# Kernel optimization log

Measured on AMD Instinct MI355X. Metric: run time of the kernel, lower is better.

## Reference

```python
import jax, jax.numpy as jnp
import numpy as np

B, T, E, H = 8, 2048, 1024, 128

def setup_inputs() -> dict:
    key = jax.random.key(0)
    kx, kq, kk, kv = jax.random.split(key, 4)
    x = jax.random.normal(kx, (B, T, E), dtype=jnp.float32)
    # Linear(E, H, bias=False) weights, stored as (E, H) so y = x @ W
    s = 1.0 / np.sqrt(E)
    Wq = jax.random.normal(kq, (E, H), dtype=jnp.float32) * s
    Wk = jax.random.normal(kk, (E, H), dtype=jnp.float32) * s
    Wv = jax.random.normal(kv, (E, H), dtype=jnp.float32) * s
    return {"x": x, "Wq": Wq, "Wk": Wk, "Wv": Wv}

def reference(x, Wq, Wk, Wv):
    # x: (B, T, E)
    Tcur = x.shape[1]
    q = jnp.einsum('bte,eh->bth', x, Wq)
    k = jnp.einsum('bte,eh->bth', x, Wk)
    v = jnp.einsum('bte,eh->bth', x, Wv)
    scores = jnp.einsum('bqh,bkh->bqk', q, k)  # (B, T, T)
    # NOTE: source multiplies by x.shape[2]**0.5 where x.shape[2] == T here
    scores = scores * jnp.sqrt(jnp.asarray(Tcur, dtype=scores.dtype))
    causal = jnp.tril(jnp.ones((Tcur, Tcur), dtype=bool))
    scores = jnp.where(causal, scores, -jnp.inf)
    attn = jax.nn.softmax(scores, axis=2)
    # dropout p=0.0 -> identity
    return jnp.einsum('bqk,bkh->bqh', attn, v)
```

## Files before the change

kernel.cpp:

```cpp
#include <hip/hip_runtime.h>
#include <hip/hip_bf16.h>
#include <math.h>

#define B_ 8
#define T_ 2048
#define E_ 1024
#define H_ 128
#define M_ (B_*T_)
#define SCALE_ 45.25483399593904f
#define SEG_ 4

typedef __attribute__((ext_vector_type(8))) short bf16x8;
typedef __attribute__((ext_vector_type(4))) float f32x4;

#define mfma16(A, Bv, C) __builtin_amdgcn_mfma_f32_16x16x32_bf16((A), (Bv), (C), 0, 0, 0)

#define FRAGW(g, kc, lane)  ((((size_t)(g)*32 + (kc))*64 + (lane))*8)
#define FRAGK(b, kt16, kc, lane) (((((size_t)(b)*128 + (kt16))*4 + (kc))*64 + (lane))*8)
#define FRAGV(b, ht, kt32, lane) (((((size_t)(b)*8 + (ht))*64 + (kt32))*64 + (lane))*8)

__device__ __forceinline__ ushort bf16_rne(float f) {
  unsigned u = __float_as_uint(f);
  u += 0x7fffu + ((u >> 16) & 1u);
  return (ushort)(u >> 16);
}
__device__ __forceinline__ float bf16_tof(ushort h) {
  return __uint_as_float(((unsigned)h) << 16);
}

__device__ __forceinline__ void lds_barrier() {
  asm volatile("s_waitcnt lgkmcnt(0)" ::: "memory");
  __builtin_amdgcn_s_barrier();
}

__global__ __launch_bounds__(256) void wsplit(
    const float* __restrict__ Wq, const float* __restrict__ Wk,
    const float* __restrict__ Wv,
    ushort* __restrict__ whT, ushort* __restrict__ wlT)
{
  const int idx  = blockIdx.x * 256 + threadIdx.x;
  const int mat  = idx >> 14;
  const int rem  = idx & 16383;
  const int nt   = rem >> 11;
  const int kc   = (rem >> 6) & 31;
  const int lane = rem & 63;
  const int quad = lane >> 4, l15 = lane & 15;
  const float* W = (mat == 0) ? Wq : (mat == 1) ? Wk : Wv;
  const int n  = nt * 16 + l15;
  const int k0 = kc * 32 + quad * 8;
  bf16x8 hv, lv;
  #pragma unroll
  for (int j = 0; j < 8; ++j) {
    const float f = W[(size_t)(k0 + j) * H_ + n];
    const ushort h = bf16_rne(f);
    hv[j] = (short)h;
    lv[j] = (short)bf16_rne(f - bf16_tof(h));
  }
  *(bf16x8*)(whT + (size_t)idx * 8) = hv;
  *(bf16x8*)(wlT + (size_t)idx * 8) = lv;
}

#define CVT8W(F0, F1, DSTOFF) do {                                            \
    const float f_[8] = {(F0).x, (F0).y, (F0).z, (F0).w,                      \
                         (F1).x, (F1).y, (F1).z, (F1).w};                     \
    bf16x8 hv_, lv_;                                                          \
    _Pragma("unroll")                                                         \
    for (int jj_ = 0; jj_ < 8; ++jj_) {                                       \
      const ushort h_ = bf16_rne(f_[jj_]);                                    \
      hv_[jj_] = (short)h_;                                                   \
      lv_[jj_] = (short)bf16_rne(f_[jj_] - bf16_tof(h_));                     \
    }                                                                         \
    *(bf16x8*)&SM[(DSTOFF) + ca * 8] = hv_;                                   \
    *(bf16x8*)&SM[(DSTOFF) + 2048 + ca * 8] = lv_;                            \
  } while (0)

#define AFRAG(CUR, HALFOFF, MT) \
    (*(const bf16x8*)&SM[(CUR)*8192 + (HALFOFF) + \
        (((MT)*4 + quad)*16 + (l15 ^ quad))*8])

#define PSTEP4(S, CUR, NXT, BHC, BLC, BHN, BLN) do {                          \
    bf16x8 ah_[4], al_[4];                                                    \
    _Pragma("unroll")                                                         \
    for (int mt_ = 0; mt_ < 4; ++mt_) {                                       \
      ah_[mt_] = AFRAG(CUR, 0,    mt_);                                       \
      al_[mt_] = AFRAG(CUR, 2048, mt_);                                       \
    }                                                                         \
    if ((S) + 1 < 16) {                                                       \
      _Pragma("unroll")                                                       \
      for (int kch_ = 0; kch_ < 2; ++kch_) {                                  \
        const int kcn_ = 2*((S)+1) + kch_;                                    \
        BHN[kch_*3+0] = *(const bf16x8*)(whT + FRAGW(gq,     kcn_, lane));    \
        BHN[kch_*3+1] = *(const bf16x8*)(whT + FRAGW(gq + 4, kcn_, lane));    \
        BHN[kch_*3+2] = *(const bf16x8*)(whT + FRAGW(gv,     kcn_, lane));    \
        BLN[kch_*2+0] = *(const bf16x8*)(wlT + FRAGW(gq,     kcn_, lane));    \
        BLN[kch_*2+1] = *(const bf16x8*)(wlT + FRAGW(gq + 4, kcn_, lane));    \
      }                                                                       \
    }                                                                         \
    float4 nx0_, nx1_, nx2_, nx3_;                                            \
    if ((S) + 2 < 16) {                                                       \
      nx0_ = *(const float4*)(xrow + 64*((S)+2));                             \
      nx1_ = *(const float4*)(xrow + 64*((S)+2) + 4);                         \
      nx2_ = *(const float4*)(xrow + 64*((S)+2) + 32);                        \
      nx3_ = *(const float4*)(xrow + 64*((S)+2) + 36);                        \
    } else { nx0_ = xf0; nx1_ = xf1; nx2_ = xf2; nx3_ = xf3; }                \
                                                     \
    __builtin_amdgcn_s_setprio(1);                                            \
    _Pragma("unroll")                                                         \
    for (int mt_ = 0; mt_ < 4; ++mt_) {                                       \
      acc[0][mt_] = mfma16(ah_[mt_], BHC[0], acc[0][mt_]);                    \
      acc[0][mt_] = mfma16(ah_[mt_], BLC[0], acc[0][mt_]);                    \
      acc[0][mt_] = mfma16(al_[mt_], BHC[0], acc[0][mt_]);                    \
      acc[1][mt_] = mfma16(ah_[mt_], BHC[1], acc[1][mt_]);                    \
      acc[1][mt_] = mfma16(ah_[mt_], BLC[1], acc[1][mt_]);                    \
      acc[1][mt_] = mfma16(al_[mt_], BHC[1], acc[1][mt_]);                    \
      acc[2][mt_] = mfma16(ah_[mt_], BHC[2], acc[2][mt_]);                    \
    }                                                                         \
    __builtin_amdgcn_s_setprio(0);                                            \
                                            \
    if ((S) + 1 < 16) {                                                       \
      CVT8W(xf0, xf1, (NXT)*8192);                                            \
      CVT8W(xf2, xf3, (NXT)*8192 + 4096);                                     \
    }                                                                         \
                                                \
    _Pragma("unroll")                                                         \
    for (int mt_ = 0; mt_ < 4; ++mt_) {                                       \
      ah_[mt_] = AFRAG(CUR, 4096, mt_);                                       \
      al_[mt_] = AFRAG(CUR, 6144, mt_);                                       \
    }                                                                         \
    __builtin_amdgcn_s_setprio(1);                                            \
    _Pragma("unroll")                                                         \
    for (int mt_ = 0; mt_ < 4; ++mt_) {                                       \
      acc[0][mt_] = mfma16(ah_[mt_], BHC[3], acc[0][mt_]);                    \
      acc[0][mt_] = mfma16(ah_[mt_], BLC[2], acc[0][mt_]);                    \
      acc[0][mt_] = mfma16(al_[mt_], BHC[3], acc[0][mt_]);                    \
      acc[1][mt_] = mfma16(ah_[mt_], BHC[4], acc[1][mt_]);                    \
      acc[1][mt_] = mfma16(ah_[mt_], BLC[3], acc[1][mt_]);                    \
      acc[1][mt_] = mfma16(al_[mt_], BHC[4], acc[1][mt_]);                    \
      acc[2][mt_] = mfma16(ah_[mt_], BHC[5], acc[2][mt_]);                    \
    }                                                                         \
    __builtin_amdgcn_s_setprio(0);                                            \
    xf0 = nx0_; xf1 = nx1_; xf2 = nx2_; xf3 = nx3_;                           \
    lds_barrier();                                                            \
  } while (0)

__global__ __launch_bounds__(256, 2) void proj_fused(
    const float* __restrict__ x,
    const ushort* __restrict__ whT, const ushort* __restrict__ wlT,
    ushort* __restrict__ qh, ushort* __restrict__ ql,
    ushort* __restrict__ kfh, ushort* __restrict__ kfl,
    ushort* __restrict__ vF)
{
  const int m0   = blockIdx.x * 64;
  const int half = blockIdx.y;
  const int tid  = threadIdx.x;
  const int wave = tid >> 6, lane = tid & 63;
  const int quad = lane >> 4, l15 = lane & 15;

  __shared__ __align__(16) ushort SM[16384];

  f32x4 acc[3][4];
  #pragma unroll
  for (int j = 0; j < 3; ++j)
    #pragma unroll
    for (int mt = 0; mt < 4; ++mt) acc[j][mt] = (f32x4){0.f, 0.f, 0.f, 0.f};

  const int arow  = tid >> 2;
  const int akoff = (tid & 3) * 8;
  const int ca    = ((arow >> 4) * 4 + (tid & 3)) * 16
                    + ((arow & 15) ^ (tid & 3));
  const int gq    = half * 8 + wave;
  const int gv    = 16 + half * 4 + wave;

  const float* xrow = x + (size_t)(m0 + arow) * E_ + akoff;

  float4 xf0, xf1, xf2, xf3;
  bf16x8 bhA[6], blA[4], bhB[6], blB[4];

  {
    const float4 a0 = *(const float4*)(xrow);
    const float4 a1 = *(const float4*)(xrow + 4);
    const float4 a2 = *(const float4*)(xrow + 32);
    const float4 a3 = *(const float4*)(xrow + 36);
    CVT8W(a0, a1, 0);
    CVT8W(a2, a3, 4096);
    xf0 = *(const float4*)(xrow + 64);
    xf1 = *(const float4*)(xrow + 68);
    xf2 = *(const float4*)(xrow + 96);
    xf3 = *(const float4*)(xrow + 100);
    #pragma unroll
    for (int kch = 0; kch < 2; ++kch) {
      bhA[kch*3+0] = *(const bf16x8*)(whT + FRAGW(gq,     kch, lane));
      bhA[kch*3+1] = *(const bf16x8*)(whT + FRAGW(gq + 4, kch, lane));
      bhA[kch*3+2] = *(const bf16x8*)(whT + FRAGW(gv,     kch, lane));
      blA[kch*2+0] = *(const bf16x8*)(wlT + FRAGW(gq,     kch, lane));
      blA[kch*2+1] = *(const bf16x8*)(wlT + FRAGW(gq + 4, kch, lane));
    }
  }
  lds_barrier();

  int s = 0;
  while (true) {
    PSTEP4(s, 0, 1, bhA, blA, bhB, blB); if (++s == 16) break;
    PSTEP4(s, 1, 0, bhB, blB, bhA, blA); if (++s == 16) break;
  }

  #pragma unroll
  for (int j = 0; j < 2; ++j) {
    const int g = gq + 4 * j;
    if (half == 0) {
      const int ncol = g * 16 + l15;
      #pragma unroll
      for (int mt = 0; mt < 4; ++mt)
        #pragma unroll
        for (int r = 0; r < 4; ++r) {
          const float a = acc[j][mt][r];
          const ushort h = bf16_rne(a);
          const size_t off = (size_t)(m0 + mt * 16 + quad * 4 + r) * H_ + ncol;
          qh[off] = h;
          ql[off] = bf16_rne(a - bf16_tof(h));
        }
    } else {
      const int hcol = (g - 8) * 16 + l15;
      const int kch  = hcol >> 5;
      const int qdh  = (hcol >> 3) & 3;
      const int jj   = hcol & 7;
      #pragma unroll
      for (int mt = 0; mt < 4; ++mt)
        #pragma unroll
        for (int r = 0; r < 4; ++r) {
          const float a = acc[j][mt][r];
          const int tg = m0 + mt * 16 + quad * 4 + r;
          const int bb = tg >> 11, tl = tg & 2047;
          const size_t ad = FRAGK(bb, tl >> 4, kch, qdh * 16 + (tl & 15)) + jj;
          const ushort h = bf16_rne(a);
          kfh[ad] = h;
          kfl[ad] = bf16_rne(a - bf16_tof(h));
        }
    }
  }
  __syncthreads();
  {
    ushort* smT = SM;
    const int lh = wave * 16 + l15;
    #pragma unroll
    for (int mt = 0; mt < 4; ++mt)
      #pragma unroll
      for (int r = 0; r < 4; ++r)
        smT[lh * 72 + mt * 16 + quad * 4 + r] = bf16_rne(acc[2][mt][r]);
    __syncthreads();
    const int bb = m0 >> 11, t0 = m0 & 2047;
    #pragma unroll
    for (int u = 0; u < 2; ++u) {
      const int c    = u * 256 + tid;
      const int lht  = c >> 7;
      const int ktl  = (c >> 6) & 1;
      const int lv   = c & 63;
      const int qv   = lv >> 4, l15v = lv & 15;
      *(bf16x8*)(vF + FRAGV(bb, half * 4 + lht, (t0 >> 5) + ktl, lv)) =
          *(const bf16x8*)&smT[(lht * 16 + l15v) * 72 + ktl * 32 + qv * 8];
    }
  }
}

__global__ __launch_bounds__(256) void attn_flash(
    const ushort* __restrict__ qh, const ushort* __restrict__ ql,
    const ushort* __restrict__ kfh, const ushort* __restrict__ kfl,
    const ushort* __restrict__ vF,
    ushort* __restrict__ Opart, float* __restrict__ mlpart)
{
  const int b    = (int)blockIdx.x & 7;
  const int seg  = (int)blockIdx.x >> 3;
  const int qt   = 31 - (int)blockIdx.y;
  const int q0   = qt * 64;
  const int tid  = threadIdx.x;
  const int wave = tid >> 6, lane = tid & 63;
  const int quad = lane >> 4, l15 = lane & 15;
  const f32x4 z4 = (f32x4){0.f, 0.f, 0.f, 0.f};

  __shared__ __align__(16) ushort SMa[12288];
  __shared__ __align__(16) unsigned smPw[1280];
  ushort* KhS = SMa;
  ushort* KlS = SMa + 4096;
  ushort* VtS = SMa + 8192;
  unsigned* pw = smPw + wave * 320;

  const int ntiles = 2 * qt + 2;
  const int cnt    = (ntiles + SEG_ - 1) >> 2;
  const int jt0    = seg * cnt;
  const int jt1    = (jt0 + cnt < ntiles) ? (jt0 + cnt) : ntiles;

  const int q0w = q0 + wave * 16;
  const int ntw = ((q0w + 15) >> 5) + 1;
  const size_t pidx = ((size_t)(b * 128 + qt * 4 + wave)) * SEG_ + seg;
  ushort* op = Opart + pidx * 2048;
  float*  ml = mlpart + pidx * 32;

  if (jt0 >= jt1) {
    const bf16x8 zz = {0, 0, 0, 0, 0, 0, 0, 0};
    #pragma unroll
    for (int u = 0; u < 4; ++u)
      *(bf16x8*)(op + lane * 32 + u * 8) = zz;
    if (lane < 32) ml[lane] = (lane & 1) ? 0.f : -1e30f;
    return;
  }

  const size_t base = (size_t)b * T_ * H_;

  const ushort* qhp = qh + base + (size_t)(q0w + l15) * H_ + quad * 8;
  const ushort* qlp = ql + base + (size_t)(q0w + l15) * H_ + quad * 8;
  bf16x8 Qh[4], Ql[4];
  #pragma unroll
  for (int c = 0; c < 4; ++c) {
    Qh[c] = *(const bf16x8*)(qhp + c * 32);
    Ql[c] = *(const bf16x8*)(qlp + c * 32);
  }

  f32x4 O[8];
  #pragma unroll
  for (int i = 0; i < 8; ++i) O[i] = z4;
  float mst = -1e30f;
  float lst = 0.f;

  bf16x8 rkh[2], rkl[2], rv[2];
  {
    #pragma unroll
    for (int u = 0; u < 2; ++u) {
      const int c = u * 256 + tid;
      rkh[u] = *(const bf16x8*)(kfh + FRAGK(b, 2 * jt0 + (c >> 8), (c >> 6) & 3, c & 63));
      rkl[u] = *(const bf16x8*)(kfl + FRAGK(b, 2 * jt0 + (c >> 8), (c >> 6) & 3, c & 63));
      rv[u]  = *(const bf16x8*)(vF  + FRAGV(b, c >> 6, jt0, c & 63));
    }
  }

  for (int jt = jt0; jt < jt1; ++jt) {
    __syncthreads();
    #pragma unroll
    for (int u = 0; u < 2; ++u) {
      const int c = u * 256 + tid;
      *(bf16x8*)&KhS[c * 8] = rkh[u];
      *(bf16x8*)&KlS[c * 8] = rkl[u];
      *(bf16x8*)&VtS[c * 8] = rv[u];
    }
    __syncthreads();

    if (jt + 1 < jt1) {
      #pragma unroll
      for (int u = 0; u < 2; ++u) {
        const int c = u * 256 + tid;
        rkh[u] = *(const bf16x8*)(kfh + FRAGK(b, 2 * (jt + 1) + (c >> 8), (c >> 6) & 3, c & 63));
        rkl[u] = *(const bf16x8*)(kfl + FRAGK(b, 2 * (jt + 1) + (c >> 8), (c >> 6) & 3, c & 63));
        rv[u]  = *(const bf16x8*)(vF  + FRAGV(b, c >> 6, jt + 1, c & 63));
      }
    }

    if (jt < ntw) {
      const int k0 = jt * 32;
      f32x4 shh0 = z4, shh1 = z4, sx0 = z4, sx1 = z4;
      #pragma unroll
      for (int c = 0; c < 4; ++c) {
        const bf16x8 kh0 = *(const bf16x8*)&KhS[(c * 64 + lane) * 8];
        const bf16x8 kh1 = *(const bf16x8*)&KhS[((4 + c) * 64 + lane) * 8];
        const bf16x8 kl0 = *(const bf16x8*)&KlS[(c * 64 + lane) * 8];
        const bf16x8 kl1 = *(const bf16x8*)&KlS[((4 + c) * 64 + lane) * 8];
        shh0 = mfma16(kh0, Qh[c], shh0);
        shh1 = mfma16(kh1, Qh[c], shh1);
        sx0  = mfma16(kl0, Qh[c], sx0);
        sx1  = mfma16(kl1, Qh[c], sx1);
        sx0  = mfma16(kh0, Ql[c], sx0);
        sx1  = mfma16(kh1, Ql[c], sx1);
      }

      float r0[4], r1[4];
      #pragma unroll
      for (int r = 0; r < 4; ++r) {
        r0[r] = shh0[r] + sx0[r];
        r1[r] = shh1[r] + sx1[r];
      }
      if (jt == ntw - 1) {
        const int base0 = q0w + l15 - k0 - quad * 4;
        #pragma unroll
        for (int r = 0; r < 4; ++r) {
          if (r > base0)      r0[r] = -1e30f;
          if (r > base0 - 16) r1[r] = -1e30f;
        }
      }

      float pm = fmaxf(fmaxf(fmaxf(r0[0], r0[1]), fmaxf(r0[2], r0[3])),
                       fmaxf(fmaxf(r1[0], r1[1]), fmaxf(r1[2], r1[3])));
      pm = fmaxf(pm, __shfl_xor(pm, 16));
      pm = fmaxf(pm, __shfl_xor(pm, 32));

      const float mnew  = fmaxf(mst, pm);
      const float alpha = __expf((mst - mnew) * SCALE_);
      mst = mnew;

      float p0[4], p1[4];
      #pragma unroll
      for (int r = 0; r < 4; ++r) {
        p0[r] = __expf((r0[r] - mnew) * SCALE_);
        p1[r] = __expf((r1[r] - mnew) * SCALE_);
      }
      float sm = ((p0[0] + p0[1]) + (p0[2] + p0[3])) +
                 ((p1[0] + p1[1]) + (p1[2] + p1[3]));
      sm += __shfl_xor(sm, 16);
      sm += __shfl_xor(sm, 32);
      lst = lst * alpha + sm;

      const unsigned w0 = (unsigned)bf16_rne(p0[0]) | ((unsigned)bf16_rne(p0[1]) << 16);
      const unsigned w1 = (unsigned)bf16_rne(p0[2]) | ((unsigned)bf16_rne(p0[3]) << 16);
      const unsigned w2 = (unsigned)bf16_rne(p1[0]) | ((unsigned)bf16_rne(p1[1]) << 16);
      const unsigned w3 = (unsigned)bf16_rne(p1[2]) | ((unsigned)bf16_rne(p1[3]) << 16);
      *(unsigned long long*)&pw[l15 * 20 + 2 * quad] =
          (unsigned long long)w0 | ((unsigned long long)w1 << 32);
      *(unsigned long long*)&pw[l15 * 20 + 8 + 2 * quad] =
          (unsigned long long)w2 | ((unsigned long long)w3 << 32);

      #pragma unroll
      for (int ct = 0; ct < 8; ++ct) {
        O[ct][0] *= alpha; O[ct][1] *= alpha;
        O[ct][2] *= alpha; O[ct][3] *= alpha;
      }
      const bf16x8 pB = *(const bf16x8*)&pw[l15 * 20 + 4 * quad];
      #pragma unroll
      for (int ct = 0; ct < 8; ++ct) {
        const bf16x8 vf = *(const bf16x8*)&VtS[(ct * 64 + lane) * 8];
        O[ct] = mfma16(vf, pB, O[ct]);
      }
    }
  }

  __syncthreads();
  {
    ushort* smO = SMa + wave * 2176;
    #pragma unroll
    for (int ct = 0; ct < 8; ++ct)
      #pragma unroll
      for (int r = 0; r < 4; ++r)
        smO[l15 * 136 + ct * 16 + quad * 4 + r] = bf16_rne(O[ct][r]);
    #pragma unroll
    for (int u = 0; u < 4; ++u) {
      const int q_ = u * 4 + quad;
      *(bf16x8*)(op + q_ * 128 + l15 * 8) =
          *(const bf16x8*)&smO[q_ * 136 + l15 * 8];
    }
  }
  if (quad == 0) {
    ml[l15 * 2]     = mst * SCALE_;
    ml[l15 * 2 + 1] = lst;
  }
}

__global__ __launch_bounds__(256) void attn_combine(
    const ushort* __restrict__ Opart, const float* __restrict__ mlpart,
    float* __restrict__ out)
{
  const int idx = blockIdx.x * 256 + threadIdx.x;
  const int c4  = idx & 31;
  const int r   = idx >> 5;
  const int t   = r & 2047;
  const int qt  = t >> 4, r16 = t & 15;
  const size_t pb = ((size_t)((r >> 11) * 128 + qt)) * SEG_;

  float m[SEG_], l[SEG_];
  #pragma unroll
  for (int s = 0; s < SEG_; ++s) {
    m[s] = mlpart[(pb + s) * 32 + r16 * 2];
    l[s] = mlpart[(pb + s) * 32 + r16 * 2 + 1];
  }
  float M = m[0];
  #pragma unroll
  for (int s = 1; s < SEG_; ++s) M = fmaxf(M, m[s]);
  float w[SEG_], L = 0.f;
  #pragma unroll
  for (int s = 0; s < SEG_; ++s) {
    w[s] = __expf(m[s] - M);
    L += l[s] * w[s];
  }
  float4 acc = make_float4(0.f, 0.f, 0.f, 0.f);
  #pragma unroll
  for (int s = 0; s < SEG_; ++s) {
    const ushort4 o = *(const ushort4*)(Opart + (pb + s) * 2048 + r16 * 128 + c4 * 4);
    acc.x += w[s] * bf16_tof(o.x);
    acc.y += w[s] * bf16_tof(o.y);
    acc.z += w[s] * bf16_tof(o.z);
    acc.w += w[s] * bf16_tof(o.w);
  }
  const float inv = 1.0f / L;
  *(float4*)(out + (size_t)r * H_ + c4 * 4) =
      make_float4(acc.x * inv, acc.y * inv, acc.z * inv, acc.w * inv);
}

extern "C" void kernel_launch(void* const* d_in, const int* in_sizes, int n_in,
                              void* d_out, int out_size, void* d_ws, size_t ws_size,
                              hipStream_t stream) {
  (void)in_sizes; (void)n_in; (void)out_size; (void)ws_size;
  const float* x  = (const float*)d_in[0];
  const float* Wq = (const float*)d_in[1];
  const float* Wk = (const float*)d_in[2];
  const float* Wv = (const float*)d_in[3];
  float* out = (float*)d_out;

  ushort* qhb = (ushort*)d_ws;
  ushort* qlb = qhb + (size_t)M_ * H_;
  ushort* kfh = qlb + (size_t)M_ * H_;
  ushort* kfl = kfh + (size_t)M_ * H_;
  ushort* vFb = kfl + (size_t)M_ * H_;
  ushort* whT = vFb + (size_t)M_ * H_;
  ushort* wlT = whT + (size_t)3 * H_ * E_;
  ushort* Opart = wlT + (size_t)3 * H_ * E_;
  float*  mlpart = (float*)(Opart + (size_t)B_ * 128 * SEG_ * 2048);

  wsplit<<<dim3(192), 256, 0, stream>>>(Wq, Wk, Wv, whT, wlT);
  proj_fused<<<dim3(M_/64, 2), 256, 0, stream>>>(x, whT, wlT,
                                                 qhb, qlb, kfh, kfl, vFb);
  attn_flash<<<dim3(B_*SEG_, 32), 256, 0, stream>>>(qhb, qlb, kfh, kfl, vFb,
                                                    Opart, mlpart);
  attn_combine<<<dim3(2048), 256, 0, stream>>>(Opart, mlpart, out);
}
```

Measured before the change: 170.0 us.

## Fuse split-KV combine into attention kernel via last-block atomic counter

Removes the separate attn_combine launch. Each attention block now fences its partial output, bumps a per-(batch, query-tile) atomic counter, and the last of the SEG_ segment blocks merges the partials and writes the final output. The counters are zeroed in the wsplit kernel. This saves one kernel launch and lets combine work overlap with other blocks, at the cost of a threadfence and atomic per block and serial combine work in the last-arriving block.

```diff
diff --git a/kernel.cpp b/kernel.cpp
--- a/kernel.cpp
+++ b/kernel.cpp
@@ -36,8 +36,10 @@
 __global__ __launch_bounds__(256) void wsplit(
     const float* __restrict__ Wq, const float* __restrict__ Wk,
     const float* __restrict__ Wv,
-    ushort* __restrict__ whT, ushort* __restrict__ wlT)
+    ushort* __restrict__ whT, ushort* __restrict__ wlT,
+    unsigned* __restrict__ cnt)
 {
+  if (blockIdx.x == 0) cnt[threadIdx.x] = 0u;
   const int idx  = blockIdx.x * 256 + threadIdx.x;
   const int mat  = idx >> 14;
   const int rem  = idx & 16383;
@@ -103,7 +105,6 @@
       nx2_ = *(const float4*)(xrow + 64*((S)+2) + 32);                        \
       nx3_ = *(const float4*)(xrow + 64*((S)+2) + 36);                        \
     } else { nx0_ = xf0; nx1_ = xf1; nx2_ = xf2; nx3_ = xf3; }                \
-                                                     \
     __builtin_amdgcn_s_setprio(1);                                            \
     _Pragma("unroll")                                                         \
     for (int mt_ = 0; mt_ < 4; ++mt_) {                                       \
@@ -116,12 +117,10 @@
       acc[2][mt_] = mfma16(ah_[mt_], BHC[2], acc[2][mt_]);                    \
     }                                                                         \
     __builtin_amdgcn_s_setprio(0);                                            \
-                                            \
     if ((S) + 1 < 16) {                                                       \
       CVT8W(xf0, xf1, (NXT)*8192);                                            \
       CVT8W(xf2, xf3, (NXT)*8192 + 4096);                                     \
     }                                                                         \
-                                                \
     _Pragma("unroll")                                                         \
     for (int mt_ = 0; mt_ < 4; ++mt_) {                                       \
       ah_[mt_] = AFRAG(CUR, 4096, mt_);                                       \
@@ -266,7 +265,8 @@
     const ushort* __restrict__ qh, const ushort* __restrict__ ql,
     const ushort* __restrict__ kfh, const ushort* __restrict__ kfl,
     const ushort* __restrict__ vF,
-    ushort* __restrict__ Opart, float* __restrict__ mlpart)
+    ushort* __restrict__ Opart, float* __restrict__ mlpart,
+    float* __restrict__ out, unsigned* __restrict__ cnt)
 {
   const int b    = (int)blockIdx.x & 7;
   const int seg  = (int)blockIdx.x >> 3;
@@ -279,15 +279,16 @@
 
   __shared__ __align__(16) ushort SMa[12288];
   __shared__ __align__(16) unsigned smPw[1280];
+  __shared__ int lastFlag;
   ushort* KhS = SMa;
   ushort* KlS = SMa + 4096;
   ushort* VtS = SMa + 8192;
   unsigned* pw = smPw + wave * 320;
 
   const int ntiles = 2 * qt + 2;
-  const int cnt    = (ntiles + SEG_ - 1) >> 2;
-  const int jt0    = seg * cnt;
-  const int jt1    = (jt0 + cnt < ntiles) ? (jt0 + cnt) : ntiles;
+  const int cntseg = (ntiles + SEG_ - 1) >> 2;
+  const int jt0    = seg * cntseg;
+  const int jt1    = (jt0 + cntseg < ntiles) ? (jt0 + cntseg) : ntiles;
 
   const int q0w = q0 + wave * 16;
   const int ntw = ((q0w + 15) >> 5) + 1;
@@ -301,193 +302,200 @@
     for (int u = 0; u < 4; ++u)
       *(bf16x8*)(op + lane * 32 + u * 8) = zz;
     if (lane < 32) ml[lane] = (lane & 1) ? 0.f : -1e30f;
-    return;
-  }
-
-  const size_t base = (size_t)b * T_ * H_;
-
-  const ushort* qhp = qh + base + (size_t)(q0w + l15) * H_ + quad * 8;
-  const ushort* qlp = ql + base + (size_t)(q0w + l15) * H_ + quad * 8;
-  bf16x8 Qh[4], Ql[4];
-  #pragma unroll
-  for (int c = 0; c < 4; ++c) {
-    Qh[c] = *(const bf16x8*)(qhp + c * 32);
-    Ql[c] = *(const bf16x8*)(qlp + c * 32);
-  }
-
-  f32x4 O[8];
-  #pragma unroll
-  for (int i = 0; i < 8; ++i) O[i] = z4;
-  float mst = -1e30f;
-  float lst = 0.f;
-
-  bf16x8 rkh[2], rkl[2], rv[2];
-  {
-    #pragma unroll
-    for (int u = 0; u < 2; ++u) {
-      const int c = u * 256 + tid;
-      rkh[u] = *(const bf16x8*)(kfh + FRAGK(b, 2 * jt0 + (c >> 8), (c >> 6) & 3, c & 63));
-      rkl[u] = *(const bf16x8*)(kfl + FRAGK(b, 2 * jt0 + (c >> 8), (c >> 6) & 3, c & 63));
-      rv[u]  = *(const bf16x8*)(vF  + FRAGV(b, c >> 6, jt0, c & 63));
-    }
-  }
-
-  for (int jt = jt0; jt < jt1; ++jt) {
-    __syncthreads();
-    #pragma unroll
-    for (int u = 0; u < 2; ++u) {
-      const int c = u * 256 + tid;
-      *(bf16x8*)&KhS[c * 8] = rkh[u];
-      *(bf16x8*)&KlS[c * 8] = rkl[u];
-      *(bf16x8*)&VtS[c * 8] = rv[u];
-    }
-    __syncthreads();
-
-    if (jt + 1 < jt1) {
+  } else {
+    const size_t base = (size_t)b * T_ * H_;
+
+    const ushort* qhp = qh + base + (size_t)(q0w + l15) * H_ + quad * 8;
+    const ushort* qlp = ql + base + (size_t)(q0w + l15) * H_ + quad * 8;
+    bf16x8 Qh[4], Ql[4];
+    #pragma unroll
+    for (int c = 0; c < 4; ++c) {
+      Qh[c] = *(const bf16x8*)(qhp + c * 32);
+      Ql[c] = *(const bf16x8*)(qlp + c * 32);
+    }
+
+    f32x4 O[8];
+    #pragma unroll
+    for (int i = 0; i < 8; ++i) O[i] = z4;
+    float mst = -1e30f;
+    float lst = 0.f;
+
+    bf16x8 rkh[2], rkl[2], rv[2];
+    {
       #pragma unroll
       for (int u = 0; u < 2; ++u) {
         const int c = u * 256 + tid;
-        rkh[u] = *(const bf16x8*)(kfh + FRAGK(b, 2 * (jt + 1) + (c >> 8), (c >> 6) & 3, c & 63));
-        rkl[u] = *(const bf16x8*)(kfl + FRAGK(b, 2 * (jt + 1) + (c >> 8), (c >> 6) & 3, c & 63));
-        rv[u]  = *(const bf16x8*)(vF  + FRAGV(b, c >> 6, jt + 1, c & 63));
-      }
-    }
-
-    if (jt < ntw) {
-      const int k0 = jt * 32;
-      f32x4 shh0 = z4, shh1 = z4, sx0 = z4, sx1 = z4;
-      #pragma unroll
-      for (int c = 0; c < 4; ++c) {
-        const bf16x8 kh0 = *(const bf16x8*)&KhS[(c * 64 + lane) * 8];
-        const bf16x8 kh1 = *(const bf16x8*)&KhS[((4 + c) * 64 + lane) * 8];
-        const bf16x8 kl0 = *(const bf16x8*)&KlS[(c * 64 + lane) * 8];
-        const bf16x8 kl1 = *(const bf16x8*)&KlS[((4 + c) * 64 + lane) * 8];
-        shh0 = mfma16(kh0, Qh[c], shh0);
-        shh1 = mfma16(kh1, Qh[c], shh1);
-        sx0  = mfma16(kl0, Qh[c], sx0);
-        sx1  = mfma16(kl1, Qh[c], sx1);
-        sx0  = mfma16(kh0, Ql[c], sx0);
-        sx1  = mfma16(kh1, Ql[c], sx1);
-      }
-
-      float r0[4], r1[4];
-      #pragma unroll
-      for (int r = 0; r < 4; ++r) {
-        r0[r] = shh0[r] + sx0[r];
-        r1[r] = shh1[r] + sx1[r];
-      }
-      if (jt == ntw - 1) {
-        const int base0 = q0w + l15 - k0 - quad * 4;
+        rkh[u] = *(const bf16x8*)(kfh + FRAGK(b, 2 * jt0 + (c >> 8), (c >> 6) & 3, c & 63));
+        rkl[u] = *(const bf16x8*)(kfl + FRAGK(b, 2 * jt0 + (c >> 8), (c >> 6) & 3, c & 63));
+        rv[u]  = *(const bf16x8*)(vF  + FRAGV(b, c >> 6, jt0, c & 63));
+      }
+    }
+
+    for (int jt = jt0; jt < jt1; ++jt) {
+      __syncthreads();
+      #pragma unroll
+      for (int u = 0; u < 2; ++u) {
+        const int c = u * 256 + tid;
+        *(bf16x8*)&KhS[c * 8] = rkh[u];
+        *(bf16x8*)&KlS[c * 8] = rkl[u];
+        *(bf16x8*)&VtS[c * 8] = rv[u];
+      }
+      __syncthreads();
+
+      if (jt + 1 < jt1) {
+        #pragma unroll
+        for (int u = 0; u < 2; ++u) {
+          const int c = u * 256 + tid;
+          rkh[u] = *(const bf16x8*)(kfh + FRAGK(b, 2 * (jt + 1) + (c >> 8), (c >> 6) & 3, c & 63));
+          rkl[u] = *(const bf16x8*)(kfl + FRAGK(b, 2 * (jt + 1) + (c >> 8), (c >> 6) & 3, c & 63));
+          rv[u]  = *(const bf16x8*)(vF  + FRAGV(b, c >> 6, jt + 1, c & 63));
+        }
+      }
+
+      if (jt < ntw) {
+        const int k0 = jt * 32;
+        f32x4 shh0 = z4, shh1 = z4, sx0 = z4, sx1 = z4;
+        #pragma unroll
+        for (int c = 0; c < 4; ++c) {
+          const bf16x8 kh0 = *(const bf16x8*)&KhS[(c * 64 + lane) * 8];
+          const bf16x8 kh1 = *(const bf16x8*)&KhS[((4 + c) * 64 + lane) * 8];
+          const bf16x8 kl0 = *(const bf16x8*)&KlS[(c * 64 + lane) * 8];
+          const bf16x8 kl1 = *(const bf16x8*)&KlS[((4 + c) * 64 + lane) * 8];
+          shh0 = mfma16(kh0, Qh[c], shh0);
+          shh1 = mfma16(kh1, Qh[c], shh1);
+          sx0  = mfma16(kl0, Qh[c], sx0);
+          sx1  = mfma16(kl1, Qh[c], sx1);
+          sx0  = mfma16(kh0, Ql[c], sx0);
+          sx1  = mfma16(kh1, Ql[c], sx1);
+        }
+
+        float r0[4], r1[4];
         #pragma unroll
         for (int r = 0; r < 4; ++r) {
-          if (r > base0)      r0[r] = -1e30f;
-          if (r > base0 - 16) r1[r] = -1e30f;
-        }
-      }
-
-      float pm = fmaxf(fmaxf(fmaxf(r0[0], r0[1]), fmaxf(r0[2], r0[3])),
-                       fmaxf(fmaxf(r1[0], r1[1]), fmaxf(r1[2], r1[3])));
-      pm = fmaxf(pm, __shfl_xor(pm, 16));
-      pm = fmaxf(pm, __shfl_xor(pm, 32));
-
-      const float mnew  = fmaxf(mst, pm);
-      const float alpha = __expf((mst - mnew) * SCALE_);
-      mst = mnew;
-
-      float p0[4], p1[4];
-      #pragma unroll
-      for (int r = 0; r < 4; ++r) {
-        p0[r] = __expf((r0[r] - mnew) * SCALE_);
-        p1[r] = __expf((r1[r] - mnew) * SCALE_);
-      }
-      float sm = ((p0[0] + p0[1]) + (p0[2] + p0[3])) +
-                 ((p1[0] + p1[1]) + (p1[2] + p1[3]));
-      sm += __shfl_xor(sm, 16);
-      sm += __shfl_xor(sm, 32);
-      lst = lst * alpha + sm;
-
-      const unsigned w0 = (unsigned)bf16_rne(p0[0]) | ((unsigned)bf16_rne(p0[1]) << 16);
-      const unsigned w1 = (unsigned)bf16_rne(p0[2]) | ((unsigned)bf16_rne(p0[3]) << 16);
-      const unsigned w2 = (unsigned)bf16_rne(p1[0]) | ((unsigned)bf16_rne(p1[1]) << 16);
-      const unsigned w3 = (unsigned)bf16_rne(p1[2]) | ((unsigned)bf16_rne(p1[3]) << 16);
-      *(unsigned long long*)&pw[l15 * 20 + 2 * quad] =
-          (unsigned long long)w0 | ((unsigned long long)w1 << 32);
-      *(unsigned long long*)&pw[l15 * 20 + 8 + 2 * quad] =
-          (unsigned long long)w2 | ((unsigned long long)w3 << 32);
-
-      #pragma unroll
-      for (int ct = 0; ct < 8; ++ct) {
-        O[ct][0] *= alpha; O[ct][1] *= alpha;
-        O[ct][2] *= alpha; O[ct][3] *= alpha;
-      }
-      const bf16x8 pB = *(const bf16x8*)&pw[l15 * 20 + 4 * quad];
-      #pragma unroll
-      for (int ct = 0; ct < 8; ++ct) {
-        const bf16x8 vf = *(const bf16x8*)&VtS[(ct * 64 + lane) * 8];
-        O[ct] = mfma16(vf, pB, O[ct]);
-      }
-    }
-  }
-
+          r0[r] = shh0[r] + sx0[r];
+          r1[r] = shh1[r] + sx1[r];
+        }
+        if (jt == ntw - 1) {
+          const int base0 = q0w + l15 - k0 - quad * 4;
+          #pragma unroll
+          for (int r = 0; r < 4; ++r) {
+            if (r > base0)      r0[r] = -1e30f;
+            if (r > base0 - 16) r1[r] = -1e30f;
+          }
+        }
+
+        float pm = fmaxf(fmaxf(fmaxf(r0[0], r0[1]), fmaxf(r0[2], r0[3])),
+                         fmaxf(fmaxf(r1[0], r1[1]), fmaxf(r1[2], r1[3])));
+        pm = fmaxf(pm, __shfl_xor(pm, 16));
+        pm = fmaxf(pm, __shfl_xor(pm, 32));
+
+        const float mnew  = fmaxf(mst, pm);
+        const float alpha = __expf((mst - mnew) * SCALE_);
+        mst = mnew;
+
+        float p0[4], p1[4];
+        #pragma unroll
+        for (int r = 0; r < 4; ++r) {
+          p0[r] = __expf((r0[r] - mnew) * SCALE_);
+          p1[r] = __expf((r1[r] - mnew) * SCALE_);
+        }
+        float sm = ((p0[0] + p0[1]) + (p0[2] + p0[3])) +
+                   ((p1[0] + p1[1]) + (p1[2] + p1[3]));
+        sm += __shfl_xor(sm, 16);
+        sm += __shfl_xor(sm, 32);
+        lst = lst * alpha + sm;
+
+        const unsigned w0 = (unsigned)bf16_rne(p0[0]) | ((unsigned)bf16_rne(p0[1]) << 16);
+        const unsigned w1 = (unsigned)bf16_rne(p0[2]) | ((unsigned)bf16_rne(p0[3]) << 16);
+        const unsigned w2 = (unsigned)bf16_rne(p1[0]) | ((unsigned)bf16_rne(p1[1]) << 16);
+        const unsigned w3 = (unsigned)bf16_rne(p1[2]) | ((unsigned)bf16_rne(p1[3]) << 16);
+        *(unsigned long long*)&pw[l15 * 20 + 2 * quad] =
+            (unsigned long long)w0 | ((unsigned long long)w1 << 32);
+        *(unsigned long long*)&pw[l15 * 20 + 8 + 2 * quad] =
+            (unsigned long long)w2 | ((unsigned long long)w3 << 32);
+
+        #pragma unroll
+        for (int ct = 0; ct < 8; ++ct) {
+          O[ct][0] *= alpha; O[ct][1] *= alpha;
+          O[ct][2] *= alpha; O[ct][3] *= alpha;
+        }
+        const bf16x8 pB = *(const bf16x8*)&pw[l15 * 20 + 4 * quad];
+        #pragma unroll
+        for (int ct = 0; ct < 8; ++ct) {
+          const bf16x8 vf = *(const bf16x8*)&VtS[(ct * 64 + lane) * 8];
+          O[ct] = mfma16(vf, pB, O[ct]);
+        }
+      }
+    }
+
+    __syncthreads();
+    {
+      ushort* smO = SMa + wave * 2176;
+      #pragma unroll
+      for (int ct = 0; ct < 8; ++ct)
+        #pragma unroll
+        for (int r = 0; r < 4; ++r)
+          smO[l15 * 136 + ct * 16 + quad * 4 + r] = bf16_rne(O[ct][r]);
+      #pragma unroll
+      for (int u = 0; u < 4; ++u) {
+        const int q_ = u * 4 + quad;
+        *(bf16x8*)(op + q_ * 128 + l15 * 8) =
+            *(const bf16x8*)&smO[q_ * 136 + l15 * 8];
+      }
+    }
+    if (quad == 0) {
+      ml[l15 * 2]     = mst * SCALE_;
+      ml[l15 * 2 + 1] = lst;
+    }
+  }
+
+  __threadfence();
   __syncthreads();
-  {
-    ushort* smO = SMa + wave * 2176;
-    #pragma unroll
-    for (int ct = 0; ct < 8; ++ct)
-      #pragma unroll
-      for (int r = 0; r < 4; ++r)
-        smO[l15 * 136 + ct * 16 + quad * 4 + r] = bf16_rne(O[ct][r]);
-    #pragma unroll
-    for (int u = 0; u < 4; ++u) {
-      const int q_ = u * 4 + quad;
-      *(bf16x8*)(op + q_ * 128 + l15 * 8) =
-          *(const bf16x8*)&smO[q_ * 136 + l15 * 8];
-    }
-  }
-  if (quad == 0) {
-    ml[l15 * 2]     = mst * SCALE_;
-    ml[l15 * 2 + 1] = lst;
-  }
-}
-
-__global__ __launch_bounds__(256) void attn_combine(
-    const ushort* __restrict__ Opart, const float* __restrict__ mlpart,
-    float* __restrict__ out)
-{
-  const int idx = blockIdx.x * 256 + threadIdx.x;
-  const int c4  = idx & 31;
-  const int r   = idx >> 5;
-  const int t   = r & 2047;
-  const int qt  = t >> 4, r16 = t & 15;
-  const size_t pb = ((size_t)((r >> 11) * 128 + qt)) * SEG_;
-
-  float m[SEG_], l[SEG_];
-  #pragma unroll
-  for (int s = 0; s < SEG_; ++s) {
-    m[s] = mlpart[(pb + s) * 32 + r16 * 2];
-    l[s] = mlpart[(pb + s) * 32 + r16 * 2 + 1];
-  }
-  float M = m[0];
-  #pragma unroll
-  for (int s = 1; s < SEG_; ++s) M = fmaxf(M, m[s]);
-  float w[SEG_], L = 0.f;
-  #pragma unroll
-  for (int s = 0; s < SEG_; ++s) {
-    w[s] = __expf(m[s] - M);
-    L += l[s] * w[s];
-  }
-  float4 acc = make_float4(0.f, 0.f, 0.f, 0.f);
-  #pragma unroll
-  for (int s = 0; s < SEG_; ++s) {
-    const ushort4 o = *(const ushort4*)(Opart + (pb + s) * 2048 + r16 * 128 + c4 * 4);
-    acc.x += w[s] * bf16_tof(o.x);
-    acc.y += w[s] * bf16_tof(o.y);
-    acc.z += w[s] * bf16_tof(o.z);
-    acc.w += w[s] * bf16_tof(o.w);
-  }
-  const float inv = 1.0f / L;
-  *(float4*)(out + (size_t)r * H_ + c4 * 4) =
-      make_float4(acc.x * inv, acc.y * inv, acc.z * inv, acc.w * inv);
+  if (tid == 0) {
+    const unsigned old = atomicAdd(&cnt[b * 32 + qt], 1u);
+    lastFlag = (old == SEG_ - 1) ? 1 : 0;
+  }
+  __syncthreads();
+  if (lastFlag) {
+    __threadfence();
+    #pragma unroll
+    for (int u = 0; u < 8; ++u) {
+      const int task = u * 256 + tid;
+      const int c4 = task & 31;
+      const int lr = task >> 5;
+      const int t  = qt * 64 + lr;
+      const int qt16 = t >> 4, r16 = t & 15;
+      const size_t pb = ((size_t)(b * 128 + qt16)) * SEG_;
+
+      float m[SEG_], l[SEG_];
+      #pragma unroll
+      for (int s = 0; s < SEG_; ++s) {
+        m[s] = mlpart[(pb + s) * 32 + r16 * 2];
+        l[s] = mlpart[(pb + s) * 32 + r16 * 2 + 1];
+      }
+      float M = m[0];
+      #pragma unroll
+      for (int s = 1; s < SEG_; ++s) M = fmaxf(M, m[s]);
+      float w[SEG_], L = 0.f;
+      #pragma unroll
+      for (int s = 0; s < SEG_; ++s) {
+        w[s] = __expf(m[s] - M);
+        L += l[s] * w[s];
+      }
+      float4 acc = make_float4(0.f, 0.f, 0.f, 0.f);
+      #pragma unroll
+      for (int s = 0; s < SEG_; ++s) {
+        const ushort4 o = *(const ushort4*)(Opart + (pb + s) * 2048 + r16 * 128 + c4 * 4);
+        acc.x += w[s] * bf16_tof(o.x);
+        acc.y += w[s] * bf16_tof(o.y);
+        acc.z += w[s] * bf16_tof(o.z);
+        acc.w += w[s] * bf16_tof(o.w);
+      }
+      const float inv = 1.0f / L;
+      *(float4*)(out + ((size_t)(b * 2048 + t)) * H_ + c4 * 4) =
+          make_float4(acc.x * inv, acc.y * inv, acc.z * inv, acc.w * inv);
+    }
+  }
 }
 
 extern "C" void kernel_launch(void* const* d_in, const int* in_sizes, int n_in,
@@ -509,11 +517,11 @@
   ushort* wlT = whT + (size_t)3 * H_ * E_;
   ushort* Opart = wlT + (size_t)3 * H_ * E_;
   float*  mlpart = (float*)(Opart + (size_t)B_ * 128 * SEG_ * 2048);
-
-  wsplit<<<dim3(192), 256, 0, stream>>>(Wq, Wk, Wv, whT, wlT);
+  unsigned* cnt  = (unsigned*)(mlpart + (size_t)B_ * 128 * SEG_ * 32);
+
+  wsplit<<<dim3(192), 256, 0, stream>>>(Wq, Wk, Wv, whT, wlT, cnt);
   proj_fused<<<dim3(M_/64, 2), 256, 0, stream>>>(x, whT, wlT,
                                                  qhb, qlb, kfh, kfl, vFb);
   attn_flash<<<dim3(B_*SEG_, 32), 256, 0, stream>>>(qhb, qlb, kfh, kfl, vFb,
-                                                    Opart, mlpart);
-  attn_combine<<<dim3(2048), 256, 0, stream>>>(Opart, mlpart, out);
-}
+                                                    Opart, mlpart, out, cnt);
+}
```

Result: slower. 292.2 us (+71.9%).

## Load K/V fragments directly from global memory, dropping LDS staging and barriers

Applied to the files above, without the earlier changes.

The flash attention kernel no longer stages K-high, K-low and V tiles through shared memory with register prefetch and two __syncthreads per tile. Each wave now reads its MFMA fragments straight from the pre-swizzled global buffers and stops its loop at its own causal limit instead of the block-wide range. This removes the block barriers and LDS traffic and lets waves proceed independently. The cost is that all four waves fetch the same K/V data redundantly from L2/L1, and the register prefetch that hid global latency is gone.

```diff
diff --git a/kernel.cpp b/kernel.cpp
--- a/kernel.cpp
+++ b/kernel.cpp
@@ -103,7 +103,6 @@
       nx2_ = *(const float4*)(xrow + 64*((S)+2) + 32);                        \
       nx3_ = *(const float4*)(xrow + 64*((S)+2) + 36);                        \
     } else { nx0_ = xf0; nx1_ = xf1; nx2_ = xf2; nx3_ = xf3; }                \
-                                                     \
     __builtin_amdgcn_s_setprio(1);                                            \
     _Pragma("unroll")                                                         \
     for (int mt_ = 0; mt_ < 4; ++mt_) {                                       \
@@ -116,12 +115,10 @@
       acc[2][mt_] = mfma16(ah_[mt_], BHC[2], acc[2][mt_]);                    \
     }                                                                         \
     __builtin_amdgcn_s_setprio(0);                                            \
-                                            \
     if ((S) + 1 < 16) {                                                       \
       CVT8W(xf0, xf1, (NXT)*8192);                                            \
       CVT8W(xf2, xf3, (NXT)*8192 + 4096);                                     \
     }                                                                         \
-                                                \
     _Pragma("unroll")                                                         \
     for (int mt_ = 0; mt_ < 4; ++mt_) {                                       \
       ah_[mt_] = AFRAG(CUR, 4096, mt_);                                       \
@@ -277,11 +274,8 @@
   const int quad = lane >> 4, l15 = lane & 15;
   const f32x4 z4 = (f32x4){0.f, 0.f, 0.f, 0.f};
 
-  __shared__ __align__(16) ushort SMa[12288];
   __shared__ __align__(16) unsigned smPw[1280];
-  ushort* KhS = SMa;
-  ushort* KlS = SMa + 4096;
-  ushort* VtS = SMa + 8192;
+  __shared__ __align__(16) ushort  smO[8704];
   unsigned* pw = smPw + wave * 320;
 
   const int ntiles = 2 * qt + 2;
@@ -321,127 +315,100 @@
   float mst = -1e30f;
   float lst = 0.f;
 
-  bf16x8 rkh[2], rkl[2], rv[2];
-  {
-    #pragma unroll
-    for (int u = 0; u < 2; ++u) {
-      const int c = u * 256 + tid;
-      rkh[u] = *(const bf16x8*)(kfh + FRAGK(b, 2 * jt0 + (c >> 8), (c >> 6) & 3, c & 63));
-      rkl[u] = *(const bf16x8*)(kfl + FRAGK(b, 2 * jt0 + (c >> 8), (c >> 6) & 3, c & 63));
-      rv[u]  = *(const bf16x8*)(vF  + FRAGV(b, c >> 6, jt0, c & 63));
-    }
-  }
-
-  for (int jt = jt0; jt < jt1; ++jt) {
-    __syncthreads();
-    #pragma unroll
-    for (int u = 0; u < 2; ++u) {
-      const int c = u * 256 + tid;
-      *(bf16x8*)&KhS[c * 8] = rkh[u];
-      *(bf16x8*)&KlS[c * 8] = rkl[u];
-      *(bf16x8*)&VtS[c * 8] = rv[u];
-    }
-    __syncthreads();
-
-    if (jt + 1 < jt1) {
-      #pragma unroll
-      for (int u = 0; u < 2; ++u) {
-        const int c = u * 256 + tid;
-        rkh[u] = *(const bf16x8*)(kfh + FRAGK(b, 2 * (jt + 1) + (c >> 8), (c >> 6) & 3, c & 63));
-        rkl[u] = *(const bf16x8*)(kfl + FRAGK(b, 2 * (jt + 1) + (c >> 8), (c >> 6) & 3, c & 63));
-        rv[u]  = *(const bf16x8*)(vF  + FRAGV(b, c >> 6, jt + 1, c & 63));
-      }
-    }
-
-    if (jt < ntw) {
-      const int k0 = jt * 32;
-      f32x4 shh0 = z4, shh1 = z4, sx0 = z4, sx1 = z4;
-      #pragma unroll
-      for (int c = 0; c < 4; ++c) {
-        const bf16x8 kh0 = *(const bf16x8*)&KhS[(c * 64 + lane) * 8];
-        const bf16x8 kh1 = *(const bf16x8*)&KhS[((4 + c) * 64 + lane) * 8];
-        const bf16x8 kl0 = *(const bf16x8*)&KlS[(c * 64 + lane) * 8];
-        const bf16x8 kl1 = *(const bf16x8*)&KlS[((4 + c) * 64 + lane) * 8];
-        shh0 = mfma16(kh0, Qh[c], shh0);
-        shh1 = mfma16(kh1, Qh[c], shh1);
-        sx0  = mfma16(kl0, Qh[c], sx0);
-        sx1  = mfma16(kl1, Qh[c], sx1);
-        sx0  = mfma16(kh0, Ql[c], sx0);
-        sx1  = mfma16(kh1, Ql[c], sx1);
-      }
-
-      float r0[4], r1[4];
+  const size_t kvb = (size_t)b * 262144;
+  const int jtc = (jt1 < ntw) ? jt1 : ntw;
+
+  for (int jt = jt0; jt < jtc; ++jt) {
+    const ushort* pKh = kfh + kvb + (size_t)jt * 4096;
+    const ushort* pKl = kfl + kvb + (size_t)jt * 4096;
+    const ushort* pV  = vF  + kvb + (size_t)jt * 512;
+    const int k0 = jt * 32;
+
+    f32x4 shh0 = z4, shh1 = z4, sx0 = z4, sx1 = z4;
+    #pragma unroll
+    for (int c = 0; c < 4; ++c) {
+      const bf16x8 kh0 = *(const bf16x8*)(pKh + c * 512 + lane * 8);
+      const bf16x8 kh1 = *(const bf16x8*)(pKh + (4 + c) * 512 + lane * 8);
+      const bf16x8 kl0 = *(const bf16x8*)(pKl + c * 512 + lane * 8);
+      const bf16x8 kl1 = *(const bf16x8*)(pKl + (4 + c) * 512 + lane * 8);
+      shh0 = mfma16(kh0, Qh[c], shh0);
+      shh1 = mfma16(kh1, Qh[c], shh1);
+      sx0  = mfma16(kl0, Qh[c], sx0);
+      sx1  = mfma16(kl1, Qh[c], sx1);
+      sx0  = mfma16(kh0, Ql[c], sx0);
+      sx1  = mfma16(kh1, Ql[c], sx1);
+    }
+
+    float r0[4], r1[4];
+    #pragma unroll
+    for (int r = 0; r < 4; ++r) {
+      r0[r] = shh0[r] + sx0[r];
+      r1[r] = shh1[r] + sx1[r];
+    }
+    if (jt == ntw - 1) {
+      const int base0 = q0w + l15 - k0 - quad * 4;
       #pragma unroll
       for (int r = 0; r < 4; ++r) {
-        r0[r] = shh0[r] + sx0[r];
-        r1[r] = shh1[r] + sx1[r];
+        if (r > base0)      r0[r] = -1e30f;
+        if (r > base0 - 16) r1[r] = -1e30f;
       }
-      if (jt == ntw - 1) {
-        const int base0 = q0w + l15 - k0 - quad * 4;
-        #pragma unroll
-        for (int r = 0; r < 4; ++r) {
-          if (r > base0)      r0[r] = -1e30f;
-          if (r > base0 - 16) r1[r] = -1e30f;
-        }
-      }
-
-      float pm = fmaxf(fmaxf(fmaxf(r0[0], r0[1]), fmaxf(r0[2], r0[3])),
-                       fmaxf(fmaxf(r1[0], r1[1]), fmaxf(r1[2], r1[3])));
-      pm = fmaxf(pm, __shfl_xor(pm, 16));
-      pm = fmaxf(pm, __shfl_xor(pm, 32));
-
-      const float mnew  = fmaxf(mst, pm);
-      const float alpha = __expf((mst - mnew) * SCALE_);
-      mst = mnew;
-
-      float p0[4], p1[4];
-      #pragma unroll
-      for (int r = 0; r < 4; ++r) {
-        p0[r] = __expf((r0[r] - mnew) * SCALE_);
-        p1[r] = __expf((r1[r] - mnew) * SCALE_);
-      }
-      float sm = ((p0[0] + p0[1]) + (p0[2] + p0[3])) +
-                 ((p1[0] + p1[1]) + (p1[2] + p1[3]));
-      sm += __shfl_xor(sm, 16);
-      sm += __shfl_xor(sm, 32);
-      lst = lst * alpha + sm;
-
-      const unsigned w0 = (unsigned)bf16_rne(p0[0]) | ((unsigned)bf16_rne(p0[1]) << 16);
-      const unsigned w1 = (unsigned)bf16_rne(p0[2]) | ((unsigned)bf16_rne(p0[3]) << 16);
-      const unsigned w2 = (unsigned)bf16_rne(p1[0]) | ((unsigned)bf16_rne(p1[1]) << 16);
-      const unsigned w3 = (unsigned)bf16_rne(p1[2]) | ((unsigned)bf16_rne(p1[3]) << 16);
-      *(unsigned long long*)&pw[l15 * 20 + 2 * quad] =
-          (unsigned long long)w0 | ((unsigned long long)w1 << 32);
-      *(unsigned long long*)&pw[l15 * 20 + 8 + 2 * quad] =
-          (unsigned long long)w2 | ((unsigned long long)w3 << 32);
-
-      #pragma unroll
-      for (int ct = 0; ct < 8; ++ct) {
-        O[ct][0] *= alpha; O[ct][1] *= alpha;
-        O[ct][2] *= alpha; O[ct][3] *= alpha;
-      }
-      const bf16x8 pB = *(const bf16x8*)&pw[l15 * 20 + 4 * quad];
-      #pragma unroll
-      for (int ct = 0; ct < 8; ++ct) {
-        const bf16x8 vf = *(const bf16x8*)&VtS[(ct * 64 + lane) * 8];
-        O[ct] = mfma16(vf, pB, O[ct]);
-      }
-    }
-  }
-
-  __syncthreads();
+    }
+
+    float pm = fmaxf(fmaxf(fmaxf(r0[0], r0[1]), fmaxf(r0[2], r0[3])),
+                     fmaxf(fmaxf(r1[0], r1[1]), fmaxf(r1[2], r1[3])));
+    pm = fmaxf(pm, __shfl_xor(pm, 16));
+    pm = fmaxf(pm, __shfl_xor(pm, 32));
+
+    const float mnew  = fmaxf(mst, pm);
+    const float alpha = __expf((mst - mnew) * SCALE_);
+    mst = mnew;
+
+    float p0[4], p1[4];
+    #pragma unroll
+    for (int r = 0; r < 4; ++r) {
+      p0[r] = __expf((r0[r] - mnew) * SCALE_);
+      p1[r] = __expf((r1[r] - mnew) * SCALE_);
+    }
+    float sm = ((p0[0] + p0[1]) + (p0[2] + p0[3])) +
+               ((p1[0] + p1[1]) + (p1[2] + p1[3]));
+    sm += __shfl_xor(sm, 16);
+    sm += __shfl_xor(sm, 32);
+    lst = lst * alpha + sm;
+
+    const unsigned w0 = (unsigned)bf16_rne(p0[0]) | ((unsigned)bf16_rne(p0[1]) << 16);
+    const unsigned w1 = (unsigned)bf16_rne(p0[2]) | ((unsigned)bf16_rne(p0[3]) << 16);
+    const unsigned w2 = (unsigned)bf16_rne(p1[0]) | ((unsigned)bf16_rne(p1[1]) << 16);
+    const unsigned w3 = (unsigned)bf16_rne(p1[2]) | ((unsigned)bf16_rne(p1[3]) << 16);
+    *(unsigned long long*)&pw[l15 * 20 + 2 * quad] =
+        (unsigned long long)w0 | ((unsigned long long)w1 << 32);
+    *(unsigned long long*)&pw[l15 * 20 + 8 + 2 * quad] =
+        (unsigned long long)w2 | ((unsigned long long)w3 << 32);
+
+    #pragma unroll
+    for (int ct = 0; ct < 8; ++ct) {
+      O[ct][0] *= alpha; O[ct][1] *= alpha;
+      O[ct][2] *= alpha; O[ct][3] *= alpha;
+    }
+    const bf16x8 pB = *(const bf16x8*)&pw[l15 * 20 + 4 * quad];
+    #pragma unroll
+    for (int ct = 0; ct < 8; ++ct) {
+      const bf16x8 vf = *(const bf16x8*)(pV + ct * 32768 + lane * 8);
+      O[ct] = mfma16(vf, pB, O[ct]);
+    }
+  }
+
   {
-    ushort* smO = SMa + wave * 2176;
+    ushort* so = smO + wave * 2176;
     #pragma unroll
     for (int ct = 0; ct < 8; ++ct)
       #pragma unroll
       for (int r = 0; r < 4; ++r)
-        smO[l15 * 136 + ct * 16 + quad * 4 + r] = bf16_rne(O[ct][r]);
+        so[l15 * 136 + ct * 16 + quad * 4 + r] = bf16_rne(O[ct][r]);
     #pragma unroll
     for (int u = 0; u < 4; ++u) {
       const int q_ = u * 4 + quad;
       *(bf16x8*)(op + q_ * 128 + l15 * 8) =
-          *(const bf16x8*)&smO[q_ * 136 + l15 * 8];
+          *(const bf16x8*)&so[q_ * 136 + l15 * 8];
     }
   }
   if (quad == 0) {
```

Measured after the change: 167.2 us. About the same (-1.7%).
